# Performance work log

Hardware: AMD Instinct MI355X
Metric: run time of the kernel (lower is better)

The kernel has to match this reference:

```python
import jax, jax.numpy as jnp
import numpy as np

RADIUS = 0.05
HMIN = -0.02
HMAXES = (0.01, 0.02, 0.03, 0.04)
NSAMPLE = 64
BN_EPS = 1e-5


def _group(d_rot, hmax):
    # d_rot: (B,S,N,3) seed-relative coords rotated into the gripper frame (d @ R)
    # Cylinder query: approach axis is x; keep first NSAMPLE points with
    # y^2+z^2 < r^2 and hmin < x < hmax; pad with first hit (0 if no hit),
    # matching the CUDA cylinder_query kernel semantics.
    N = d_rot.shape[2]
    h = d_rot[..., 0]
    r2 = d_rot[..., 1] ** 2 + d_rot[..., 2] ** 2
    mask = (r2 < RADIUS * RADIUS) & (h > HMIN) & (h < hmax)
    key = jnp.where(mask, jnp.arange(N, dtype=jnp.int32), N)
    neg_top, _ = jax.lax.top_k(-key, NSAMPLE)   # ascending keys = first hits in point order
    idx = -neg_top                               # (B,S,k); == N where slot is invalid
    first = idx[..., :1]
    idx = jnp.where(idx < N, idx, jnp.where(first < N, first, 0))
    return jnp.take_along_axis(d_rot, idx[..., None], axis=2)  # (B,S,k,3)


def _mlp_layer(x, w, b, g, be, m, v):
    # 1x1 Conv2d + BatchNorm (eval-mode, running stats) + ReLU, as in pt_utils.SharedMLP
    x = jnp.einsum('bcpn,oc->bopn', x, w) + b[None, :, None, None]
    scale = g / jnp.sqrt(v + BN_EPS)
    x = (x - m[None, :, None, None]) * scale[None, :, None, None] + be[None, :, None, None]
    return jax.nn.relu(x)


def _forward(seed_xyz, pointcloud, vp_rot, params):
    B, S, _ = seed_xyz.shape
    D = len(HMAXES)
    d = pointcloud[:, None, :, :] - seed_xyz[:, :, None, :]          # (B,S,N,3)
    d_rot = jnp.einsum('bsnc,bscd->bsnd', d, vp_rot)                 # rotate into gripper frame
    groups = jnp.stack([_group(d_rot, h) for h in HMAXES], axis=2)   # (B,S,D,k,3)
    x = groups.transpose(0, 4, 1, 2, 3).reshape(B, 3, S * D, NSAMPLE)  # (B,3,S*D,k)
    for (w, b, g, be, m, v) in params:
        x = _mlp_layer(x, w, b, g, be, m, v)
    x = x.max(axis=-1)                                               # max-pool over nsample
    return x.reshape(B, -1, S, D)                                    # (B,256,S,D)


def setup_inputs() -> dict:
    key = jax.random.key(0)
    ks = jax.random.split(key, 8)
    B, S, N = 2, 1024, 16384
    inp = {
        'seed_xyz': jax.random.uniform(ks[0], (B, S, 3), jnp.float32),
        'pointcloud': jax.random.uniform(ks[1], (B, N, 3), jnp.float32),
        'vp_rot': jax.random.normal(ks[2], (B, S, 3, 3), jnp.float32),
    }
    dims = [3, 64, 128, 256]
    for i in range(3):
        cin, cout = dims[i], dims[i + 1]
        k1, k2, k3, k4, k5, k6 = jax.random.split(ks[3 + i], 6)
        inp[f'w{i+1}'] = jax.random.normal(k1, (cout, cin), jnp.float32) * 0.05
        inp[f'b{i+1}'] = jax.random.normal(k2, (cout,), jnp.float32) * 0.01
        inp[f'g{i+1}'] = 1.0 + 0.1 * jax.random.normal(k3, (cout,), jnp.float32)
        inp[f'be{i+1}'] = jax.random.normal(k4, (cout,), jnp.float32) * 0.01
        inp[f'm{i+1}'] = jax.random.normal(k5, (cout,), jnp.float32) * 0.01
        inp[f'v{i+1}'] = jax.random.uniform(k6, (cout,), jnp.float32, 0.5, 1.5)
    return inp


def reference(seed_xyz, pointcloud, vp_rot,
              w1, b1, g1, be1, m1, v1,
              w2, b2, g2, be2, m2, v2,
              w3, b3, g3, be3, m3, v3):
    params = [(w1, b1, g1, be1, m1, v1),
              (w2, b2, g2, be2, m2, v2),
              (w3, b3, g3, be3, m3, v3)]
    return _forward(seed_xyz, pointcloud, vp_rot, params)
```

## Files before the change

kernel.cpp:

```cpp
#include <hip/hip_runtime.h>
#include <hip/hip_bf16.h>
#include <cstdint>
#include <cstddef>

#define NSAMP  64
#define NPT    16384
#define NLVL   4
#define NCHUNK 8
#define CHSZ   (NPT / NCHUNK)

typedef __attribute__((ext_vector_type(8))) short  short8;
typedef __attribute__((ext_vector_type(4))) float  floatx4;
typedef __attribute__((ext_vector_type(4))) unsigned int uintx4;
typedef __attribute__((ext_vector_type(2))) unsigned int uintx2;

__device__ __forceinline__ unsigned short f2bf(float x) {
    union { float f; unsigned int u; } c; c.f = x;
    unsigned int r = (c.u + 0x7fffu + ((c.u >> 16) & 1u)) >> 16;
    return (unsigned short)r;
}
__device__ __forceinline__ unsigned int f2bf2(float a, float b) {
    __hip_bfloat162 t = __float22bfloat162_rn(make_float2(a, b));
    union { __hip_bfloat162 h; unsigned int u; } c; c.h = t;
    return c.u;
}

__global__ __launch_bounds__(256) void prep_kernel(
    const float* __restrict__ w1, const float* __restrict__ b1, const float* __restrict__ g1,
    const float* __restrict__ be1, const float* __restrict__ m1, const float* __restrict__ v1,
    const float* __restrict__ w2, const float* __restrict__ b2, const float* __restrict__ g2,
    const float* __restrict__ be2, const float* __restrict__ m2, const float* __restrict__ v2,
    const float* __restrict__ w3, const float* __restrict__ b3, const float* __restrict__ g3,
    const float* __restrict__ be3, const float* __restrict__ m3, const float* __restrict__ v3,
    float* __restrict__ w1f, float* __restrict__ fb1,
    unsigned short* __restrict__ w2b, float* __restrict__ fb2,
    unsigned short* __restrict__ w3b, float* __restrict__ fb3)
{
    const int t  = blockIdx.x * 256 + threadIdx.x;
    const int nt = gridDim.x * 256;
    const float eps = 1e-5f;
    for (int i = t; i < 64 * 3; i += nt)    w1f[i] = w1[i] * (g1[i / 3] / sqrtf(v1[i / 3] + eps));
    for (int i = t; i < 64; i += nt)        fb1[i] = (b1[i] - m1[i]) * (g1[i] / sqrtf(v1[i] + eps)) + be1[i];
    for (int i = t; i < 128 * 64; i += nt)  w2b[i] = f2bf(w2[i] * (g2[i / 64] / sqrtf(v2[i / 64] + eps)));
    for (int i = t; i < 128; i += nt)       fb2[i] = (b2[i] - m2[i]) * (g2[i] / sqrtf(v2[i] + eps)) + be2[i];
    for (int i = t; i < 256 * 128; i += nt) w3b[i] = f2bf(w3[i] * (g3[i / 128] / sqrtf(v3[i / 128] + eps)));
    for (int i = t; i < 256; i += nt)       fb3[i] = (b3[i] - m3[i]) * (g3[i] / sqrtf(v3[i] + eps)) + be3[i];
}

__global__ __launch_bounds__(512) void scan_kernel(
    const float* __restrict__ seedp, const float* __restrict__ pc,
    const float* __restrict__ rot, unsigned short* __restrict__ buf,
    int* __restrict__ cnts)
{
    __shared__ float ch[CHSZ * 3];
    const int tid  = threadIdx.x;
    const int lane = tid & 63;
    const int w    = tid >> 6;
    const int sg   = blockIdx.x >> 3;
    const int c    = blockIdx.x & 7;
    const int g    = sg * 8 + w;
    const int b    = g >> 10;

    {
        const float4* src = (const float4*)(pc + ((size_t)b * NPT + c * CHSZ) * 3);
        float4* dst = (float4*)ch;
        dst[tid]        = src[tid];
        dst[tid + 512]  = src[tid + 512];
        dst[tid + 1024] = src[tid + 1024];
    }
    __syncthreads();

    const float* sd = seedp + (size_t)g * 3;
    const float sx = sd[0], sy = sd[1], sz = sd[2];
    const float* R = rot + (size_t)g * 9;
    const float r00 = R[0], r01 = R[1], r02 = R[2];
    const float r10 = R[3], r11 = R[4], r12 = R[5];
    const float r20 = R[6], r21 = R[7], r22 = R[8];
    const float nc0 = -(sx * r00 + sy * r10 + sz * r20);
    const float nc1 = -(sx * r01 + sy * r11 + sz * r21);
    const float nc2 = -(sx * r02 + sy * r12 + sz * r22);

    unsigned short* bufg = buf + (size_t)g * (NLVL * NCHUNK * 64);
    int cnt0 = 0, cnt1 = 0, cnt2 = 0, cnt3 = 0;
    const unsigned long long lm = (1ull << lane) - 1ull;

    for (int bt = 0; bt < 4; ++bt) {
        float pxv[8], pyv[8], pzv[8];
        #pragma unroll
        for (int j = 0; j < 8; ++j) {
            const int pl = (bt * 8 + j) * 64 + lane;
            pxv[j] = ch[pl * 3];
            pyv[j] = ch[pl * 3 + 1];
            pzv[j] = ch[pl * 3 + 2];
        }
        #pragma unroll
        for (int j = 0; j < 8; ++j) {
            const float h = fmaf(pxv[j], r00, fmaf(pyv[j], r10, fmaf(pzv[j], r20, nc0)));
            const float u = fmaf(pxv[j], r01, fmaf(pyv[j], r11, fmaf(pzv[j], r21, nc1)));
            const float v = fmaf(pxv[j], r02, fmaf(pyv[j], r12, fmaf(pzv[j], r22, nc2)));
            const float r2 = fmaf(u, u, v * v);
            const bool base = (r2 < 0.0025f) && (h > -0.02f) && (h < 0.04f);

            const unsigned long long bal3 = __ballot(base);
            if (bal3 == 0ull) continue;

            const unsigned short pidx = (unsigned short)(c * CHSZ + (bt * 8 + j) * 64 + lane);
            #pragma unroll
            for (int l = 0; l < NLVL; ++l) {
                unsigned long long bal; bool m;
                if (l == 3) { m = base; bal = bal3; }
                else {
                    const float hm = (l == 0) ? 0.01f : (l == 1) ? 0.02f : 0.03f;
                    m = base && (h < hm);
                    bal = __ballot(m);
                }
                int& cnt = (l == 0) ? cnt0 : (l == 1) ? cnt1 : (l == 2) ? cnt2 : cnt3;
                if (m) {
                    const int pos = cnt + (int)__popcll(bal & lm);
                    if (pos < 64) bufg[(l * NCHUNK + c) * 64 + pos] = pidx;
                }
                cnt += (int)__popcll(bal);
            }
        }
        if (cnt0 >= NSAMP) break;
    }

    if (lane == 0) {
        int* cg = cnts + (size_t)g * (NLVL * NCHUNK);
        cg[0 * NCHUNK + c] = cnt0;
        cg[1 * NCHUNK + c] = cnt1;
        cg[2 * NCHUNK + c] = cnt2;
        cg[3 * NCHUNK + c] = cnt3;
    }
}

__global__ __launch_bounds__(256) void gather_kernel(
    const float* __restrict__ seedp, const float* __restrict__ pc,
    const float* __restrict__ rot,
    const unsigned short* __restrict__ buf, const int* __restrict__ cnts,
    float* __restrict__ gx)
{
    const int n = threadIdx.x & 63;
    const int W = blockIdx.x * 4 + (threadIdx.x >> 6);
    const int g = W >> 2, l = W & 3;
    const int b = g >> 10;

    const int* cg = cnts + (size_t)g * (NLVL * NCHUNK) + l * NCHUNK;
    const unsigned short* bl = buf + (size_t)g * (NLVL * NCHUNK * 64) + l * (NCHUNK * 64);
    int idx = -1, acc = 0, firstIdx = -1;
    #pragma unroll
    for (int c = 0; c < NCHUNK; ++c) {
        const int cn = min(cg[c], 64);
        if (cn > 0 && firstIdx < 0) firstIdx = (int)bl[c * 64];
        if (n >= acc && n < acc + cn) idx = (int)bl[c * 64 + (n - acc)];
        acc += cn;
    }
    if (idx < 0) idx = (firstIdx >= 0) ? firstIdx : 0;

    const float* sd = seedp + (size_t)g * 3;
    const float* R  = rot   + (size_t)g * 9;
    const float* pp = pc + ((size_t)b * NPT + idx) * 3;
    const float dx = pp[0] - sd[0], dy = pp[1] - sd[1], dz = pp[2] - sd[2];

    float* o = gx + (size_t)W * 192;
    o[n]       = dx * R[0] + dy * R[3] + dz * R[6];
    o[64 + n]  = dx * R[1] + dy * R[4] + dz * R[7];
    o[128 + n] = dx * R[2] + dy * R[5] + dz * R[8];
}

__global__ __launch_bounds__(256) void mlp_kernel(
    const float* __restrict__ gx,
    const float* __restrict__ w1f, const float* __restrict__ fb1,
    const unsigned short* __restrict__ w2b, const float* __restrict__ fb2,
    const unsigned short* __restrict__ w3b, const float* __restrict__ fb3,
    float* __restrict__ out)
{
    __shared__ unsigned short h1t[4096];
    __shared__ unsigned short h2t[8192];

    const int tid = threadIdx.x;
    const int n      = tid & 63;
    const int w      = tid >> 6;
    const int lane15 = tid & 15;
    const int quad   = (tid & 63) >> 4;

    short8 wa3[4][4];
    float  wb3[4];
    #pragma unroll
    for (int mt = 0; mt < 4; ++mt) {
        const int m0 = (w * 4 + mt) * 16;
        #pragma unroll
        for (int k0 = 0; k0 < 4; ++k0)
            wa3[mt][k0] = *(const short8*)&w3b[(m0 + lane15) * 128 + k0 * 32 + quad * 8];
        wb3[mt] = fb3[m0 + lane15];
    }

    short8 a20[2], a21[2]; floatx4 b2v[2];
    #pragma unroll
    for (int mi = 0; mi < 2; ++mi) {
        const int m0 = (w * 2 + mi) * 16;
        a20[mi] = *(const short8*)&w2b[(m0 + lane15) * 64 + quad * 8];
        a21[mi] = *(const short8*)&w2b[(m0 + lane15) * 64 + 32 + quad * 8];
        b2v[mi] = *(const floatx4*)&fb2[m0 + quad * 4];
    }

    {
        const float* xb = gx + (size_t)(blockIdx.x * 4) * 192;
        const float x0 = xb[n], x1 = xb[64 + n], x2 = xb[128 + n];
        unsigned int p[8];
        #pragma unroll
        for (int j = 0; j < 8; ++j) {
            const int o0 = __builtin_amdgcn_readfirstlane(w * 16 + 2 * j);
            const float a0 = fb1[o0]     + w1f[o0*3]*x0   + w1f[o0*3+1]*x1 + w1f[o0*3+2]*x2;
            const float a1 = fb1[o0 + 1] + w1f[o0*3+3]*x0 + w1f[o0*3+4]*x1 + w1f[o0*3+5]*x2;
            p[j] = f2bf2(fmaxf(a0, 0.f), fmaxf(a1, 0.f));
        }
        *(uintx4*)&h1t[(((w * 2)    ) * 64 + n) * 8] = (uintx4){p[0], p[1], p[2], p[3]};
        *(uintx4*)&h1t[(((w * 2) + 1) * 64 + n) * 8] = (uintx4){p[4], p[5], p[6], p[7]};
    }

    for (int it = 0; it < 4; ++it) {
        const int gp = blockIdx.x * 4 + it;
        const int g = gp >> 2, l = gp & 3;
        const int b = g >> 10, s = g & 1023;

        __syncthreads();

        {
            short8 bfr[4][2];
            #pragma unroll
            for (int nt = 0; nt < 4; ++nt)
                #pragma unroll
                for (int k0 = 0; k0 < 2; ++k0)
                    bfr[nt][k0] = *(const short8*)&h1t[((k0 * 4 + quad) * 64 + nt * 16 + lane15) * 8];

            #pragma unroll
            for (int mi = 0; mi < 2; ++mi) {
                const int m0 = (w * 2 + mi) * 16;
                #pragma unroll
                for (int nt = 0; nt < 4; ++nt) {
                    floatx4 acc = b2v[mi];
                    acc = __builtin_amdgcn_mfma_f32_16x16x32_bf16(a20[mi], bfr[nt][0], acc, 0, 0, 0);
                    acc = __builtin_amdgcn_mfma_f32_16x16x32_bf16(a21[mi], bfr[nt][1], acc, 0, 0, 0);
                    const int n2 = nt * 16 + lane15;
                    const unsigned int q0 = f2bf2(fmaxf(acc[0], 0.f), fmaxf(acc[1], 0.f));
                    const unsigned int q1 = f2bf2(fmaxf(acc[2], 0.f), fmaxf(acc[3], 0.f));
                    const int kb = (m0 >> 3) + (quad >> 1);
                    *(uintx2*)&h2t[(kb * 64 + n2) * 8 + (quad & 1) * 4] = (uintx2){q0, q1};
                }
            }
        }
        __syncthreads();

        short8 bfr3[4][4];
        #pragma unroll
        for (int nt = 0; nt < 4; ++nt)
            #pragma unroll
            for (int k0 = 0; k0 < 4; ++k0)
                bfr3[nt][k0] = *(const short8*)&h2t[((k0 * 4 + quad) * 64 + nt * 16 + lane15) * 8];

        if (it < 3) {
            const float* xb = gx + (size_t)(gp + 1) * 192;
            const float x0 = xb[n], x1 = xb[64 + n], x2 = xb[128 + n];
            unsigned int p[8];
            #pragma unroll
            for (int j = 0; j < 8; ++j) {
                const int o0 = __builtin_amdgcn_readfirstlane(w * 16 + 2 * j);
                const float a0 = fb1[o0]     + w1f[o0*3]*x0   + w1f[o0*3+1]*x1 + w1f[o0*3+2]*x2;
                const float a1 = fb1[o0 + 1] + w1f[o0*3+3]*x0 + w1f[o0*3+4]*x1 + w1f[o0*3+5]*x2;
                p[j] = f2bf2(fmaxf(a0, 0.f), fmaxf(a1, 0.f));
            }
            *(uintx4*)&h1t[(((w * 2)    ) * 64 + n) * 8] = (uintx4){p[0], p[1], p[2], p[3]};
            *(uintx4*)&h1t[(((w * 2) + 1) * 64 + n) * 8] = (uintx4){p[4], p[5], p[6], p[7]};
        }

        #pragma unroll
        for (int mt = 0; mt < 4; ++mt) {
            const int m0 = (w * 4 + mt) * 16;
            floatx4 acc[4];
            #pragma unroll
            for (int nt = 0; nt < 4; ++nt) acc[nt] = (floatx4){0.f, 0.f, 0.f, 0.f};
            #pragma unroll
            for (int k0 = 0; k0 < 4; ++k0)
                #pragma unroll
                for (int nt = 0; nt < 4; ++nt)
                    acc[nt] = __builtin_amdgcn_mfma_f32_16x16x32_bf16(bfr3[nt][k0], wa3[mt][k0], acc[nt], 0, 0, 0);

            float t0 = fmaxf(fmaxf(acc[0][0], acc[0][1]), fmaxf(acc[0][2], acc[0][3]));
            float t1 = fmaxf(fmaxf(acc[1][0], acc[1][1]), fmaxf(acc[1][2], acc[1][3]));
            float t2 = fmaxf(fmaxf(acc[2][0], acc[2][1]), fmaxf(acc[2][2], acc[2][3]));
            float t3 = fmaxf(fmaxf(acc[3][0], acc[3][1]), fmaxf(acc[3][2], acc[3][3]));
            float t  = fmaxf(fmaxf(t0, t1), fmaxf(t2, t3));
            t = fmaxf(t, __shfl_xor(t, 16));
            t = fmaxf(t, __shfl_xor(t, 32));
            if (quad == 0) {
                const int o = m0 + lane15;
                out[(((size_t)b * 256 + o) * 1024 + s) * 4 + l] = fmaxf(t + wb3[mt], 0.f);
            }
        }
    }
}

extern "C" void kernel_launch(void* const* d_in, const int* in_sizes, int n_in,
                              void* d_out, int out_size, void* d_ws, size_t ws_size,
                              hipStream_t stream) {
    const float* seed = (const float*)d_in[0];
    const float* pc   = (const float*)d_in[1];
    const float* rot  = (const float*)d_in[2];
    const float* w1 = (const float*)d_in[3];
    const float* b1 = (const float*)d_in[4];
    const float* g1 = (const float*)d_in[5];
    const float* be1 = (const float*)d_in[6];
    const float* m1 = (const float*)d_in[7];
    const float* v1 = (const float*)d_in[8];
    const float* w2 = (const float*)d_in[9];
    const float* b2 = (const float*)d_in[10];
    const float* g2 = (const float*)d_in[11];
    const float* be2 = (const float*)d_in[12];
    const float* m2 = (const float*)d_in[13];
    const float* v2 = (const float*)d_in[14];
    const float* w3 = (const float*)d_in[15];
    const float* b3 = (const float*)d_in[16];
    const float* g3 = (const float*)d_in[17];
    const float* be3 = (const float*)d_in[18];
    const float* m3 = (const float*)d_in[19];
    const float* v3 = (const float*)d_in[20];

    float* w1f = (float*)d_ws;
    float* fb1 = w1f + 192;
    float* fb2 = fb1 + 64;
    float* fb3 = fb2 + 128;
    unsigned short* w2b = (unsigned short*)(fb3 + 256);
    unsigned short* w3b = w2b + 8192;
    unsigned short* buf = w3b + 32768;
    int* cnts = (int*)(buf + 4194304);
    float* gx = (float*)(cnts + 65536);

    prep_kernel<<<64, 256, 0, stream>>>(w1, b1, g1, be1, m1, v1,
                                        w2, b2, g2, be2, m2, v2,
                                        w3, b3, g3, be3, m3, v3,
                                        w1f, fb1, w2b, fb2, w3b, fb3);
    scan_kernel<<<2048, 512, 0, stream>>>(seed, pc, rot, buf, cnts);
    gather_kernel<<<2048, 256, 0, stream>>>(seed, pc, rot, buf, cnts, gx);
    mlp_kernel<<<2048, 256, 0, stream>>>(gx, w1f, fb1, w2b, fb2, w3b, fb3,
                                         (float*)d_out);
}
```

Before: 185.3 us.

## Stream layer weights from global per iteration to cut register pressure

Drops the register-resident layer-2 and layer-3 weight fragments and the full bfr3 tile. Weights are now reloaded from global/L2 each iteration, with software prefetch of the next m-tile's layer-3 weights, and the layer-3 GEMM is split into two N-halves that keep a running max. Launch bounds now request 5 waves per SIMD to raise occupancy. The trade-off is more global load traffic (cached weights) and extra address arithmetic, in exchange for fewer VGPRs and more concurrent blocks.

```diff
diff --git a/kernel.cpp b/kernel.cpp
--- a/kernel.cpp
+++ b/kernel.cpp
@@ -168,7 +168,7 @@
     o[128 + n] = dx * R[2] + dy * R[5] + dz * R[8];
 }
 
-__global__ __launch_bounds__(256) void mlp_kernel(
+__global__ __launch_bounds__(256, 5) void mlp_kernel(
     const float* __restrict__ gx,
     const float* __restrict__ w1f, const float* __restrict__ fb1,
     const unsigned short* __restrict__ w2b, const float* __restrict__ fb2,
@@ -184,26 +184,6 @@
     const int lane15 = tid & 15;
     const int quad   = (tid & 63) >> 4;
 
-    short8 wa3[4][4];
-    float  wb3[4];
-    #pragma unroll
-    for (int mt = 0; mt < 4; ++mt) {
-        const int m0 = (w * 4 + mt) * 16;
-        #pragma unroll
-        for (int k0 = 0; k0 < 4; ++k0)
-            wa3[mt][k0] = *(const short8*)&w3b[(m0 + lane15) * 128 + k0 * 32 + quad * 8];
-        wb3[mt] = fb3[m0 + lane15];
-    }
-
-    short8 a20[2], a21[2]; floatx4 b2v[2];
-    #pragma unroll
-    for (int mi = 0; mi < 2; ++mi) {
-        const int m0 = (w * 2 + mi) * 16;
-        a20[mi] = *(const short8*)&w2b[(m0 + lane15) * 64 + quad * 8];
-        a21[mi] = *(const short8*)&w2b[(m0 + lane15) * 64 + 32 + quad * 8];
-        b2v[mi] = *(const floatx4*)&fb2[m0 + quad * 4];
-    }
-
     {
         const float* xb = gx + (size_t)(blockIdx.x * 4) * 192;
         const float x0 = xb[n], x1 = xb[64 + n], x2 = xb[128 + n];
@@ -237,11 +217,14 @@
             #pragma unroll
             for (int mi = 0; mi < 2; ++mi) {
                 const int m0 = (w * 2 + mi) * 16;
+                const short8 a0 = *(const short8*)&w2b[(m0 + lane15) * 64 + quad * 8];
+                const short8 a1 = *(const short8*)&w2b[(m0 + lane15) * 64 + 32 + quad * 8];
+                const floatx4 bv = *(const floatx4*)&fb2[m0 + quad * 4];
                 #pragma unroll
                 for (int nt = 0; nt < 4; ++nt) {
-                    floatx4 acc = b2v[mi];
-                    acc = __builtin_amdgcn_mfma_f32_16x16x32_bf16(a20[mi], bfr[nt][0], acc, 0, 0, 0);
-                    acc = __builtin_amdgcn_mfma_f32_16x16x32_bf16(a21[mi], bfr[nt][1], acc, 0, 0, 0);
+                    floatx4 acc = bv;
+                    acc = __builtin_amdgcn_mfma_f32_16x16x32_bf16(a0, bfr[nt][0], acc, 0, 0, 0);
+                    acc = __builtin_amdgcn_mfma_f32_16x16x32_bf16(a1, bfr[nt][1], acc, 0, 0, 0);
                     const int n2 = nt * 16 + lane15;
                     const unsigned int q0 = f2bf2(fmaxf(acc[0], 0.f), fmaxf(acc[1], 0.f));
                     const unsigned int q1 = f2bf2(fmaxf(acc[2], 0.f), fmaxf(acc[3], 0.f));
@@ -252,13 +235,6 @@
         }
         __syncthreads();
 
-        short8 bfr3[4][4];
-        #pragma unroll
-        for (int nt = 0; nt < 4; ++nt)
-            #pragma unroll
-            for (int k0 = 0; k0 < 4; ++k0)
-                bfr3[nt][k0] = *(const short8*)&h2t[((k0 * 4 + quad) * 64 + nt * 16 + lane15) * 8];
-
         if (it < 3) {
             const float* xb = gx + (size_t)(gp + 1) * 192;
             const float x0 = xb[n], x1 = xb[64 + n], x2 = xb[128 + n];
@@ -274,28 +250,54 @@
             *(uintx4*)&h1t[(((w * 2) + 1) * 64 + n) * 8] = (uintx4){p[4], p[5], p[6], p[7]};
         }
 
+        float tmax[4] = {-3.4e38f, -3.4e38f, -3.4e38f, -3.4e38f};
+        #pragma unroll
+        for (int half = 0; half < 2; ++half) {
+            short8 bfr3[2][4];
+            #pragma unroll
+            for (int ntl = 0; ntl < 2; ++ntl) {
+                const int nt = half * 2 + ntl;
+                #pragma unroll
+                for (int k0 = 0; k0 < 4; ++k0)
+                    bfr3[ntl][k0] = *(const short8*)&h2t[((k0 * 4 + quad) * 64 + nt * 16 + lane15) * 8];
+            }
+            short8 wf[4];
+            #pragma unroll
+            for (int k0 = 0; k0 < 4; ++k0)
+                wf[k0] = *(const short8*)&w3b[((w * 4) * 16 + lane15) * 128 + k0 * 32 + quad * 8];
+
+            #pragma unroll
+            for (int mt = 0; mt < 4; ++mt) {
+                short8 wc[4];
+                #pragma unroll
+                for (int k0 = 0; k0 < 4; ++k0) wc[k0] = wf[k0];
+                if (mt < 3) {
+                    const int m0n = (w * 4 + mt + 1) * 16;
+                    #pragma unroll
+                    for (int k0 = 0; k0 < 4; ++k0)
+                        wf[k0] = *(const short8*)&w3b[(m0n + lane15) * 128 + k0 * 32 + quad * 8];
+                }
+                floatx4 acc0 = (floatx4){0.f, 0.f, 0.f, 0.f};
+                floatx4 acc1 = (floatx4){0.f, 0.f, 0.f, 0.f};
+                #pragma unroll
+                for (int k0 = 0; k0 < 4; ++k0) {
+                    acc0 = __builtin_amdgcn_mfma_f32_16x16x32_bf16(bfr3[0][k0], wc[k0], acc0, 0, 0, 0);
+                    acc1 = __builtin_amdgcn_mfma_f32_16x16x32_bf16(bfr3[1][k0], wc[k0], acc1, 0, 0, 0);
+                }
+                const float t0 = fmaxf(fmaxf(acc0[0], acc0[1]), fmaxf(acc0[2], acc0[3]));
+                const float t1 = fmaxf(fmaxf(acc1[0], acc1[1]), fmaxf(acc1[2], acc1[3]));
+                tmax[mt] = fmaxf(tmax[mt], fmaxf(t0, t1));
+            }
+        }
+
         #pragma unroll
         for (int mt = 0; mt < 4; ++mt) {
-            const int m0 = (w * 4 + mt) * 16;
-            floatx4 acc[4];
-            #pragma unroll
-            for (int nt = 0; nt < 4; ++nt) acc[nt] = (floatx4){0.f, 0.f, 0.f, 0.f};
-            #pragma unroll
-            for (int k0 = 0; k0 < 4; ++k0)
-                #pragma unroll
-                for (int nt = 0; nt < 4; ++nt)
-                    acc[nt] = __builtin_amdgcn_mfma_f32_16x16x32_bf16(bfr3[nt][k0], wa3[mt][k0], acc[nt], 0, 0, 0);
-
-            float t0 = fmaxf(fmaxf(acc[0][0], acc[0][1]), fmaxf(acc[0][2], acc[0][3]));
-            float t1 = fmaxf(fmaxf(acc[1][0], acc[1][1]), fmaxf(acc[1][2], acc[1][3]));
-            float t2 = fmaxf(fmaxf(acc[2][0], acc[2][1]), fmaxf(acc[2][2], acc[2][3]));
-            float t3 = fmaxf(fmaxf(acc[3][0], acc[3][1]), fmaxf(acc[3][2], acc[3][3]));
-            float t  = fmaxf(fmaxf(t0, t1), fmaxf(t2, t3));
+            float t = tmax[mt];
             t = fmaxf(t, __shfl_xor(t, 16));
             t = fmaxf(t, __shfl_xor(t, 32));
             if (quad == 0) {
-                const int o = m0 + lane15;
-                out[(((size_t)b * 256 + o) * 1024 + s) * 4 + l] = fmaxf(t + wb3[mt], 0.f);
+                const int o = (w * 4 + mt) * 16 + lane15;
+                out[(((size_t)b * 256 + o) * 1024 + s) * 4 + l] = fmaxf(t + fb3[o], 0.f);
             }
         }
     }
```

Result: slower. 377.4 us (+103.6%).
